# Kernel tuning notes

Hardware: AMD Instinct MI355X
Metric: run time of the kernel (lower is better)

## Reference

```python
import jax, jax.numpy as jnp
import numpy as np

EMB = 128
EDGE = 32
STEPS = 3


def _lrelu(x):
    return jax.nn.leaky_relu(x, negative_slope=0.01)


def setup_inputs() -> dict:
    key = jax.random.key(0)
    ks = jax.random.split(key, 16)
    N, E, G = 50000, 400000, 256
    x = jax.random.normal(ks[0], (N, EMB), jnp.float32)
    edge_attr = jax.random.normal(ks[1], (E, EDGE), jnp.float32)
    edge_index = jax.random.randint(ks[2], (2, E), 0, N, jnp.int64)
    batch_ind = jnp.sort(jax.random.randint(ks[3], (N,), 0, G, jnp.int64))
    data_lens = jax.random.randint(ks[4], (G,), 0, G, jnp.int64)
    s = 1.0 / np.sqrt(EMB)
    Wm = jax.random.normal(ks[5], (STEPS, EMB + EDGE, EMB), jnp.float32) * s
    bm = jnp.zeros((STEPS, EMB), jnp.float32)
    Wa = jax.random.normal(ks[6], (STEPS, 3 * EMB, EMB), jnp.float32) * s
    ba = jnp.zeros((STEPS, EMB), jnp.float32)
    Wgate = jax.random.normal(ks[7], (STEPS, EMB), jnp.float32) * s
    bgate = jnp.zeros((STEPS,), jnp.float32)
    Wfeat = jax.random.normal(ks[8], (STEPS, EMB, EMB), jnp.float32) * s
    bfeat = jnp.zeros((STEPS, EMB), jnp.float32)
    Wt = jax.random.normal(ks[9], (STEPS, 2 * EMB, EMB), jnp.float32) * s
    bt = jnp.zeros((STEPS, EMB), jnp.float32)
    return {"x": x, "edge_attr": edge_attr, "Wm": Wm, "bm": bm, "Wa": Wa,
            "ba": ba, "Wgate": Wgate, "bgate": bgate, "Wfeat": Wfeat,
            "bfeat": bfeat, "Wt": Wt, "bt": bt, "edge_index": edge_index,
            "batch_ind": batch_ind, "num_graphs": 256, "data_lens": data_lens}


def reference(x, edge_attr, Wm, bm, Wa, ba, Wgate, bgate, Wfeat, bfeat, Wt, bt,
              edge_index, batch_ind, num_graphs, data_lens):
    N = x.shape[0]
    src, dst = edge_index[0], edge_index[1]  # PyG: x_j = x[src], aggregate at dst
    xg = jnp.zeros((num_graphs, EMB), x.dtype)  # xg_init is None -> zeros
    for s in range(STEPS):
        # GraphNet: gather -> message MLP -> scatter-max -> update MLP + residual
        xg_node = xg[batch_ind]                                   # [N, emb]
        z = jnp.concatenate([x[src], edge_attr], axis=1)          # [E, emb+edge]
        m = _lrelu(z @ Wm[s] + bm[s])                             # [E, emb]
        agg = jax.ops.segment_max(m, dst, num_segments=N)         # [N, emb]
        agg = jnp.where(jnp.isneginf(agg), 0.0, agg)              # PyG fills empty with 0
        z2 = jnp.concatenate([x, xg_node, agg], axis=1)           # [N, 3*emb]
        x = _lrelu(z2 @ Wa[s] + ba[s]) + x
        # GlobalNode: segment-softmax attention pooling + transform + residual
        gate = x @ Wgate[s] + bgate[s]                            # [N]
        gmax = jax.ops.segment_max(gate, batch_ind, num_segments=num_graphs)
        gmax = jnp.where(jnp.isneginf(gmax), 0.0, gmax)
        e = jnp.exp(gate - gmax[batch_ind])
        denom = jax.ops.segment_sum(e, batch_ind, num_segments=num_graphs)
        alpha = e / denom[batch_ind]                              # [N]
        feat = _lrelu(x @ Wfeat[s] + bfeat[s])                    # [N, emb]
        pooled = jax.ops.segment_sum(alpha[:, None] * feat, batch_ind,
                                     num_segments=num_graphs)     # [G, emb]
        cat = jnp.concatenate([pooled, xg], axis=1)               # [G, 2*emb]
        xg = _lrelu(cat @ Wt[s] + bt[s]) + xg
    return x, xg
```

## Files before the change

### kernel.cpp

```cpp
#include <hip/hip_runtime.h>
#include <hip/hip_bf16.h>

#define EMB 128
#define EDGE 32
#define STEPS 3

typedef short bf8s __attribute__((ext_vector_type(8)));
typedef float f32x4 __attribute__((ext_vector_type(4)));

__device__ __forceinline__ float lrelu(float v) { return v > 0.0f ? v : 0.01f * v; }
__device__ __forceinline__ unsigned short f2bf(float f) {
    unsigned u = __float_as_uint(f);
    u += 0x7fffu + ((u >> 16) & 1u);
    return (unsigned short)(u >> 16);
}
__device__ __forceinline__ float bf2f(unsigned short s) {
    return __uint_as_float(((unsigned)s) << 16);
}
__device__ __forceinline__ unsigned pk2bf(float x, float y) {
    __hip_bfloat162 h = __float22bfloat162_rn(make_float2(x, y));
    return *(unsigned*)&h;
}

__global__ void k_hist(const int* __restrict__ dst, int E, int* __restrict__ deg) {
    int e = blockIdx.x * 256 + threadIdx.x;
    if (e < E) atomicAdd(&deg[dst[e]], 1);
}

__global__ void k_scan1(const int* __restrict__ deg, int N, int* __restrict__ rowptr,
                        int* __restrict__ bsums) {
    __shared__ int s[256];
    int t = threadIdx.x;
    int i = blockIdx.x * 256 + t;
    int v = (i < N) ? deg[i] : 0;
    s[t] = v;
    __syncthreads();
#pragma unroll
    for (int off = 1; off < 256; off <<= 1) {
        int x = (t >= off) ? s[t - off] : 0;
        __syncthreads();
        s[t] += x;
        __syncthreads();
    }
    if (i < N) rowptr[i] = s[t] - v;
    if (t == 255) bsums[blockIdx.x] = s[255];
}

__global__ void k_scan2(int* __restrict__ bsums, int NB) {
    __shared__ int s[256];
    __shared__ int carry;
    int t = threadIdx.x;
    if (t == 0) carry = 0;
    __syncthreads();
    for (int base = 0; base < NB; base += 256) {
        int i = base + t;
        int v = (i < NB) ? bsums[i] : 0;
        s[t] = v;
        __syncthreads();
#pragma unroll
        for (int off = 1; off < 256; off <<= 1) {
            int x = (t >= off) ? s[t - off] : 0;
            __syncthreads();
            s[t] += x;
            __syncthreads();
        }
        int excl = s[t] - v + carry;
        if (i < NB) bsums[i] = excl;
        int tot = s[255];
        __syncthreads();
        if (t == 0) carry += tot;
        __syncthreads();
    }
}

__global__ void k_scan3(int* __restrict__ rowptr, const int* __restrict__ bsums,
                        int* __restrict__ cursor, int N, int E) {
    int i = blockIdx.x * 256 + threadIdx.x;
    if (i < N) {
        int v = rowptr[i] + bsums[i >> 8];
        rowptr[i] = v;
        cursor[i] = v;
    }
    if (i == 0) rowptr[N] = E;
}

__global__ void k_fill(const int* __restrict__ src, const int* __restrict__ dst, int E,
                       int* __restrict__ cursor, int2* __restrict__ sp2) {
    int e = blockIdx.x * 256 + threadIdx.x;
    if (e >= E) return;
    int d = dst[e];
    int p = atomicAdd(&cursor[d], 1);
    sp2[p] = make_int2(src[e], e);
}

__global__ __launch_bounds__(256) void k_eaperm(const float* __restrict__ ea,
                                                const int2* __restrict__ sp2,
                                                unsigned short* __restrict__ ea16p,
                                                int* __restrict__ srcp, int E) {
    int p = blockIdx.x * 256 + threadIdx.x;
    if (p >= E) return;
    int2 sp = sp2[p];
    srcp[p] = sp.x;
    const float4* er = (const float4*)(ea + (size_t)sp.y * EDGE);
    union { unsigned u[16]; int4 v[4]; } o;
#pragma unroll
    for (int q = 0; q < 8; ++q) {
        float4 v = er[q];
        o.u[2 * q]     = pk2bf(v.x, v.y);
        o.u[2 * q + 1] = pk2bf(v.z, v.w);
    }
    int4* dp = (int4*)(ea16p + (size_t)p * EDGE);
#pragma unroll
    for (int q = 0; q < 4; ++q) dp[q] = o.v[q];
}

__global__ __launch_bounds__(256) void k_setup(const float* __restrict__ x0,
                                               unsigned short* __restrict__ x16,
                                               int N, int XB, int NB,
                                               const float* __restrict__ ba,
                                               float* __restrict__ gb,
                                               float* __restrict__ xg_a,
                                               const int* __restrict__ batch,
                                               int* __restrict__ gstart, int G,
                                               unsigned short* __restrict__ h16,
                                               int* __restrict__ deg) {
    int b = blockIdx.x, t = threadIdx.x;
    if (b < XB) {
        size_t idx = ((size_t)b * 256 + t) * 8;
        if (idx < (size_t)N * EMB) {
            const float4* s = (const float4*)(x0 + idx);
            float4 v0 = s[0], v1 = s[1];
            union { bf8s v; unsigned u[4]; } o;
            o.u[0] = pk2bf(v0.x, v0.y);
            o.u[1] = pk2bf(v0.z, v0.w);
            o.u[2] = pk2bf(v1.x, v1.y);
            o.u[3] = pk2bf(v1.z, v1.w);
            *(bf8s*)(x16 + idx) = o.v;
        }
        return;
    }
    b -= XB;
    if (b < NB) {
        int i = b * 256 + t;
        if (i < N) deg[i] = 0;
        return;
    }
    b -= NB;
    if (b < G) {
        if (t < EMB) gb[(size_t)b * EMB + t] = ba[t];
        else xg_a[(size_t)b * EMB + (t - EMB)] = 0.f;
        if (t == 0) {
            int lo = 0, hi = N;
            while (lo < hi) {
                int mid = (lo + hi) >> 1;
                if (batch[mid] < b) lo = mid + 1; else hi = mid;
            }
            gstart[b] = lo;
        }
        return;
    }
    if (t < EMB) h16[(size_t)N * EMB + t] = 0xFF80u;
    if (t == EMB) gstart[G] = N;
}

__global__ __launch_bounds__(256) void k_wpack(const float* __restrict__ Wm,
                                               const float* __restrict__ Wa,
                                               const float* __restrict__ Wfeat,
                                               unsigned short* __restrict__ wpack) {
    int gid = blockIdx.x * 256 + threadIdx.x;
    int unit = gid >> 14;
    int e = gid & 16383;
    int s = unit / 5, u = unit % 5;
    const float* src; int rows;
    switch (u) {
        case 0: src = Wm + (size_t)s * 160 * EMB;             rows = 128; break;
        case 1: src = Wm + (size_t)s * 160 * EMB + 128 * EMB; rows = 32;  break;
        case 2: src = Wa + (size_t)s * 384 * EMB;             rows = 128; break;
        case 3: src = Wa + (size_t)s * 384 * EMB + 256 * EMB; rows = 128; break;
        default: src = Wfeat + (size_t)s * EMB * EMB;         rows = 128; break;
    }
    int k = e >> 7, n = e & 127;
    if (k >= rows) return;
    unsigned short b = f2bf(src[(size_t)k * EMB + n]);
    int kc = k >> 5, c = n >> 4, lane = (n & 15) | (((k & 31) >> 3) << 4), j = k & 7;
    wpack[(size_t)unit * 16384 + ((size_t)(kc * 8 + c) * 64 + lane) * 8 + j] = b;
}

__device__ __forceinline__ void loadAa(const unsigned short* __restrict__ A16, int row0,
                                       int wv, int lane, int N, bf8s af[4]) {
    int li = lane & 15, oct = lane >> 4;
    int m = row0 + wv * 16 + li;
    if (m >= N) m = N - 1;
    const bf8s* ar = (const bf8s*)(A16 + (size_t)m * EMB);
#pragma unroll
    for (int kc = 0; kc < 4; ++kc) af[kc] = ar[kc * 4 + oct];
}
__device__ __forceinline__ void stageB(const unsigned short* __restrict__ Bp,
                                       unsigned short* lB, int tid) {
#pragma unroll
    for (int i = 0; i < 8; ++i) {
        int idx = tid + i * 256;
        ((int4*)lB)[idx] = ((const int4*)Bp)[idx];
    }
}
__device__ __forceinline__ void mfma128r(const bf8s af[4], const unsigned short* lB,
                                         f32x4 acc[8], int lane) {
#pragma unroll
    for (int kc = 0; kc < 4; ++kc) {
#pragma unroll
        for (int c = 0; c < 8; ++c) {
            bf8s b = *(const bf8s*)&lB[((kc * 8 + c) * 64 + lane) * 8];
            acc[c] = __builtin_amdgcn_mfma_f32_16x16x32_bf16(af[kc], b, acc[c], 0, 0, 0);
        }
    }
}

__global__ __launch_bounds__(256) void k_gemm_bias(const unsigned short* __restrict__ A16,
                                                   const unsigned short* __restrict__ Bp,
                                                   const float* __restrict__ bias,
                                                   unsigned short* __restrict__ C, int N) {
    __shared__ unsigned short lB[16384];
    int tid = threadIdx.x, wv = tid >> 6, lane = tid & 63;
    int row0 = blockIdx.x * 64;
    stageB(Bp, lB, tid);
    bf8s af[4];
    loadAa(A16, row0, wv, lane, N, af);
    __syncthreads();
    f32x4 acc[8];
#pragma unroll
    for (int c = 0; c < 8; ++c) acc[c] = (f32x4){0.f, 0.f, 0.f, 0.f};
    mfma128r(af, lB, acc, lane);
    int li = lane & 15, quad = lane >> 4;
    float bcol[8];
#pragma unroll
    for (int c = 0; c < 8; ++c) bcol[c] = bias[c * 16 + li];
#pragma unroll
    for (int rr = 0; rr < 4; ++rr) {
        int m = row0 + wv * 16 + quad * 4 + rr;
        if (m < N) {
            union { bf8s v; unsigned u[4]; } o;
#pragma unroll
            for (int j = 0; j < 4; ++j)
                o.u[j] = pk2bf(acc[2 * j][rr] + bcol[2 * j],
                               acc[2 * j + 1][rr] + bcol[2 * j + 1]);
            *(bf8s*)&C[(size_t)m * EMB + li * 8] = o.v;
        }
    }
}

__global__ __launch_bounds__(256) void k_gemm_node(const float* __restrict__ x,
                                                   unsigned short* __restrict__ x16,
                                                   const unsigned short* __restrict__ agg16,
                                                   const unsigned short* __restrict__ BpX,
                                                   const unsigned short* __restrict__ BpA,
                                                   const float* __restrict__ gb,
                                                   const int* __restrict__ batch,
                                                   float* __restrict__ xout,
                                                   const float* __restrict__ wg,
                                                   const float* __restrict__ bg,
                                                   float* __restrict__ gate, int N) {
    __shared__ unsigned short lB[16384];
    int tid = threadIdx.x, wv = tid >> 6, lane = tid & 63;
    int row0 = blockIdx.x * 64;
    stageB(BpX, lB, tid);
    bf8s af[4];
    loadAa(x16, row0, wv, lane, N, af);
    __syncthreads();
    f32x4 acc[8];
#pragma unroll
    for (int c = 0; c < 8; ++c) acc[c] = (f32x4){0.f, 0.f, 0.f, 0.f};
    mfma128r(af, lB, acc, lane);
    __syncthreads();
    stageB(BpA, lB, tid);
    loadAa(agg16, row0, wv, lane, N, af);
    __syncthreads();
    mfma128r(af, lB, acc, lane);
    int li = lane & 15, quad = lane >> 4;
    float gpart[4] = {0.f, 0.f, 0.f, 0.f};
#pragma unroll
    for (int c = 0; c < 8; ++c) {
        int col = c * 16 + li;
        float wgc = wg[col];
#pragma unroll
        for (int rr = 0; rr < 4; ++rr) {
            int m = row0 + wv * 16 + quad * 4 + rr;
            if (m < N) {
                int g = batch[m];
                float b = gb[(size_t)g * EMB + col];
                float res = x[(size_t)m * EMB + col];
                float v = lrelu(acc[c][rr] + b) + res;
                xout[(size_t)m * EMB + col] = v;
                x16[(size_t)m * EMB + col] = f2bf(v);
                gpart[rr] = fmaf(v, wgc, gpart[rr]);
            }
        }
    }
#pragma unroll
    for (int rr = 0; rr < 4; ++rr) {
#pragma unroll
        for (int off = 1; off < 16; off <<= 1)
            gpart[rr] += __shfl_xor(gpart[rr], off, 64);
    }
    if (li == 0) {
        float b0 = bg[0];
#pragma unroll
        for (int rr = 0; rr < 4; ++rr) {
            int m = row0 + wv * 16 + quad * 4 + rr;
            if (m < N) gate[m] = gpart[rr] + b0;
        }
    }
}

__global__ __launch_bounds__(256) void k_gemm_feat(const unsigned short* __restrict__ A16,
                                                   const unsigned short* __restrict__ Bp,
                                                   const float* __restrict__ bias,
                                                   const float* __restrict__ gate,
                                                   const float* __restrict__ gmax,
                                                   const float* __restrict__ denom,
                                                   const int* __restrict__ batch,
                                                   float* __restrict__ pooled, int N) {
    __shared__ unsigned short lB[16384];
    int tid = threadIdx.x, wv = tid >> 6, lane = tid & 63;
    int row0 = blockIdx.x * 64;
    stageB(Bp, lB, tid);
    bf8s af[4];
    loadAa(A16, row0, wv, lane, N, af);
    __syncthreads();
    f32x4 acc[8];
#pragma unroll
    for (int c = 0; c < 8; ++c) acc[c] = (f32x4){0.f, 0.f, 0.f, 0.f};
    mfma128r(af, lB, acc, lane);
    int li = lane & 15, quad = lane >> 4;
    int rb = row0 + wv * 16;
    if (rb >= N) return;
    float alpha[4];
    int grow[4];
#pragma unroll
    for (int rr = 0; rr < 4; ++rr) {
        int m = rb + quad * 4 + rr;
        if (m < N) {
            int g = batch[m];
            grow[rr] = g;
            alpha[rr] = __expf(gate[m] - gmax[g]) / denom[g];
        } else { alpha[rr] = 0.f; grow[rr] = 0; }
    }
    int gs = batch[rb];
    int mlast = rb + 15; if (mlast >= N) mlast = N - 1;
    bool uni = (gs == batch[mlast]);
#pragma unroll
    for (int c = 0; c < 8; ++c) {
        int col = c * 16 + li;
        float b = bias[col];
        float v0 = alpha[0] * lrelu(acc[c][0] + b);
        float v1 = alpha[1] * lrelu(acc[c][1] + b);
        float v2 = alpha[2] * lrelu(acc[c][2] + b);
        float v3 = alpha[3] * lrelu(acc[c][3] + b);
        if (uni) {
            float s = (v0 + v1) + (v2 + v3);
            s += __shfl_xor(s, 16, 64);
            s += __shfl_xor(s, 32, 64);
            if (quad == 0) atomicAdd(&pooled[(size_t)gs * EMB + col], s);
        } else {
            if (rb + quad * 4 + 0 < N) atomicAdd(&pooled[(size_t)grow[0] * EMB + col], v0);
            if (rb + quad * 4 + 1 < N) atomicAdd(&pooled[(size_t)grow[1] * EMB + col], v1);
            if (rb + quad * 4 + 2 < N) atomicAdd(&pooled[(size_t)grow[2] * EMB + col], v2);
            if (rb + quad * 4 + 3 < N) atomicAdd(&pooled[(size_t)grow[3] * EMB + col], v3);
        }
    }
}

__global__ __launch_bounds__(256) void k_gseg(const float* __restrict__ gate,
                                              const int* __restrict__ gstart,
                                              float* __restrict__ gmax,
                                              float* __restrict__ denom,
                                              float* __restrict__ pooled) {
    int g = blockIdx.x;
    int t = threadIdx.x;
    if (t < EMB) pooled[(size_t)g * EMB + t] = 0.f;
    int s0 = gstart[g], s1 = gstart[g + 1];
    __shared__ float red[256];
    float mx = -__builtin_inff();
    for (int i = s0 + t; i < s1; i += 256) mx = fmaxf(mx, gate[i]);
    red[t] = mx;
    __syncthreads();
#pragma unroll
    for (int off = 128; off; off >>= 1) {
        if (t < off) red[t] = fmaxf(red[t], red[t + off]);
        __syncthreads();
    }
    float m = red[0];
    __syncthreads();
    float sum = 0.f;
    for (int i = s0 + t; i < s1; i += 256) sum += __expf(gate[i] - m);
    red[t] = sum;
    __syncthreads();
#pragma unroll
    for (int off = 128; off; off >>= 1) {
        if (t < off) red[t] += red[t + off];
        __syncthreads();
    }
    if (t == 0) {
        gmax[g] = (s1 > s0) ? m : 0.f;
        denom[g] = red[0];
    }
}

__global__ __launch_bounds__(128) void k_xg(const float* __restrict__ pooled,
                                            const float* __restrict__ xg,
                                            const float* __restrict__ Wt,
                                            const float* __restrict__ bt,
                                            float* __restrict__ xg_out,
                                            const float* __restrict__ WaGn,
                                            const float* __restrict__ ban,
                                            float* __restrict__ gb) {
    int g = blockIdx.x, c = threadIdx.x;
    __shared__ float row[256];
    row[c] = pooled[(size_t)g * EMB + c];
    row[c + 128] = xg[(size_t)g * EMB + c];
    __syncthreads();
    float acc = bt[c];
#pragma unroll 8
    for (int k = 0; k < 256; ++k) acc = fmaf(row[k], Wt[(size_t)k * EMB + c], acc);
    float v = lrelu(acc) + row[c + 128];
    xg_out[(size_t)g * EMB + c] = v;
    if (WaGn) {
        __syncthreads();
        row[c] = v;
        __syncthreads();
        float a2 = ban[c];
#pragma unroll 8
        for (int k = 0; k < EMB; ++k) a2 = fmaf(row[k], WaGn[(size_t)k * EMB + c], a2);
        gb[(size_t)g * EMB + c] = a2;
    }
}

__global__ __launch_bounds__(1024) void k_fagg(const unsigned short* __restrict__ h,
                                               const unsigned short* __restrict__ ea16p,
                                               const int* __restrict__ srcp,
                                               const int* __restrict__ rowptr,
                                               const unsigned short* __restrict__ Bp,
                                               unsigned short* __restrict__ agg, int N) {
    __shared__ unsigned short lB[4096];
    int tid = threadIdx.x;
    if (tid < 512) ((int4*)lB)[tid] = ((const int4*)Bp)[tid];
    __syncthreads();
    int wv = tid >> 6, lane = tid & 63;
    int n = blockIdx.x * 16 + wv;
    if (n >= N) return;
    int li = lane & 15, oct = lane >> 4;
    int r0 = rowptr[n], r1 = rowptr[n + 1], deg = r1 - r0;

    float vm[8];
#pragma unroll
    for (int ci = 0; ci < 8; ++ci) vm[ci] = -__builtin_inff();

    for (int b = 0; b < deg; b += 16) {
        int p = r0 + b + li;
        if (p > r1 - 1) p = r1 - 1;
        int srcv = srcp[p];
        bf8s a = *(const bf8s*)&ea16p[(size_t)p * EDGE + oct * 8];
        union { bf8s v; unsigned short s[8]; } hv[4];
#pragma unroll
        for (int rr = 0; rr < 4; ++rr) {
            int sr = __shfl(srcv, oct * 4 + rr, 16);
            if (b + oct * 4 + rr >= deg) sr = N;
            hv[rr].v = *(const bf8s*)&h[(size_t)sr * EMB + li * 8];
        }
#pragma unroll
        for (int ci = 0; ci < 8; ++ci) {
            bf8s bb = *(const bf8s*)&lB[(ci * 64 + lane) * 8];
            f32x4 acc;
            acc[0] = bf2f(hv[0].s[ci]);
            acc[1] = bf2f(hv[1].s[ci]);
            acc[2] = bf2f(hv[2].s[ci]);
            acc[3] = bf2f(hv[3].s[ci]);
            acc = __builtin_amdgcn_mfma_f32_16x16x32_bf16(a, bb, acc, 0, 0, 0);
#pragma unroll
            for (int rr = 0; rr < 4; ++rr) vm[ci] = fmaxf(vm[ci], acc[rr]);
        }
    }
#pragma unroll
    for (int ci = 0; ci < 8; ++ci) {
        vm[ci] = fmaxf(vm[ci], __shfl_xor(vm[ci], 16, 64));
        vm[ci] = fmaxf(vm[ci], __shfl_xor(vm[ci], 32, 64));
    }
    float s0 = (oct == 0) ? vm[0] : (oct == 1) ? vm[1] : (oct == 2) ? vm[2] : vm[3];
    float s1 = (oct == 0) ? vm[4] : (oct == 1) ? vm[5] : (oct == 2) ? vm[6] : vm[7];
    s0 = lrelu(s0);
    s1 = lrelu(s1);
    if (deg == 0) { s0 = 0.f; s1 = 0.f; }
    agg[(size_t)n * EMB + oct * 16 + li]        = f2bf(s0);
    agg[(size_t)n * EMB + (oct + 4) * 16 + li]  = f2bf(s1);
}

extern "C" void kernel_launch(void* const* d_in, const int* in_sizes, int n_in,
                              void* d_out, int out_size, void* d_ws, size_t ws_size,
                              hipStream_t stream) {
    const float* x0    = (const float*)d_in[0];
    const float* ea    = (const float*)d_in[1];
    const float* Wm    = (const float*)d_in[2];
    const float* bm    = (const float*)d_in[3];
    const float* Wa    = (const float*)d_in[4];
    const float* ba    = (const float*)d_in[5];
    const float* Wgate = (const float*)d_in[6];
    const float* bgate = (const float*)d_in[7];
    const float* Wfeat = (const float*)d_in[8];
    const float* bfeat = (const float*)d_in[9];
    const float* Wt    = (const float*)d_in[10];
    const float* bt    = (const float*)d_in[11];
    const int*   eidx  = (const int*)d_in[12];
    const int*   batch = (const int*)d_in[13];

    int N = in_sizes[0] / EMB;
    int E = in_sizes[1] / EDGE;
    int G = in_sizes[15];

    char* w = (char*)d_ws;
    auto alloc = [&](size_t bytes) {
        char* p = w;
        w += (bytes + 255) & ~(size_t)255;
        return p;
    };
    unsigned short* h16   = (unsigned short*)alloc((size_t)(N + 1) * EMB * 2);
    unsigned short* x16   = (unsigned short*)alloc((size_t)N * EMB * 2);
    unsigned short* agg16 = (unsigned short*)alloc((size_t)N * EMB * 2);
    float* gate   = (float*)alloc((size_t)N * 4);
    float* gb     = (float*)alloc((size_t)G * EMB * 4);
    float* pooled = (float*)alloc((size_t)G * EMB * 4);
    float* gmax   = (float*)alloc((size_t)G * 4);
    float* denom  = (float*)alloc((size_t)G * 4);
    float* xg_a   = (float*)alloc((size_t)G * EMB * 4);
    float* xg_b   = (float*)alloc((size_t)G * EMB * 4);
    int* deg      = (int*)alloc((size_t)N * 4);
    int* rowptr   = (int*)alloc((size_t)(N + 1) * 4);
    int* cursor   = (int*)alloc((size_t)N * 4);
    int2* sp2     = (int2*)alloc((size_t)E * 8);
    int* srcp     = (int*)alloc((size_t)E * 4);
    unsigned short* ea16p = (unsigned short*)alloc((size_t)E * EDGE * 2);
    int* gstart   = (int*)alloc((size_t)(G + 1) * 4);
    int* bsums    = (int*)alloc(1024 * 4);
    unsigned short* wpack = (unsigned short*)alloc((size_t)15 * 16384 * 2);

    const int* esrc = eidx;
    const int* edst = eidx + E;
    int ebl = (E + 255) / 256;
    int NB  = (N + 255) / 256;
    int XB  = ((size_t)N * EMB / 8 + 255) / 256;

    k_setup<<<XB + NB + G + 1, 256, 0, stream>>>(x0, x16, N, XB, NB, ba, gb, xg_a,
                                                 batch, gstart, G, h16, deg);
    k_hist<<<ebl, 256, 0, stream>>>(edst, E, deg);
    k_scan1<<<NB, 256, 0, stream>>>(deg, N, rowptr, bsums);
    k_scan2<<<1, 256, 0, stream>>>(bsums, NB);
    k_scan3<<<NB, 256, 0, stream>>>(rowptr, bsums, cursor, N, E);
    k_fill<<<ebl, 256, 0, stream>>>(esrc, edst, E, cursor, sp2);
    k_eaperm<<<ebl, 256, 0, stream>>>(ea, sp2, ea16p, srcp, E);
    k_wpack<<<960, 256, 0, stream>>>(Wm, Wa, Wfeat, wpack);

    int gemm_blocks = (N + 63) / 64;
    int fagg_blocks = (N + 15) / 16;

    const float* x_in = x0;
    float* xg_cur = xg_a;
    float* xg_nxt = xg_b;

    for (int s = 0; s < STEPS; ++s) {
        const unsigned short* wp = wpack + (size_t)s * 5 * 16384;
        float* x_out = (s == STEPS - 1) ? (float*)d_out : (float*)x_in;

        k_gemm_bias<<<gemm_blocks, 256, 0, stream>>>(x16, wp + 0 * 16384, bm + s * EMB,
                                                     h16, N);
        k_fagg<<<fagg_blocks, 1024, 0, stream>>>(h16, ea16p, srcp, rowptr, wp + 1 * 16384,
                                                 agg16, N);
        k_gemm_node<<<gemm_blocks, 256, 0, stream>>>(x_in, x16, agg16, wp + 2 * 16384,
                                                     wp + 3 * 16384, gb, batch, x_out,
                                                     Wgate + s * EMB, bgate + s, gate, N);
        k_gseg<<<G, 256, 0, stream>>>(gate, gstart, gmax, denom, pooled);
        k_gemm_feat<<<gemm_blocks, 256, 0, stream>>>(x16, wp + 4 * 16384, bfeat + s * EMB,
                                                     gate, gmax, denom, batch, pooled, N);
        const float* WaGn = (s < STEPS - 1) ? Wa + (size_t)(s + 1) * 384 * EMB + 128 * EMB
                                            : nullptr;
        const float* ban  = (s < STEPS - 1) ? ba + (s + 1) * EMB : nullptr;
        k_xg<<<G, 128, 0, stream>>>(pooled, xg_cur, Wt + (size_t)s * 256 * EMB,
                                    bt + s * EMB, xg_nxt, WaGn, ban, gb);

        x_in = x_out;
        float* tmp = xg_cur; xg_cur = xg_nxt; xg_nxt = tmp;
    }

    hipMemcpyAsync((float*)d_out + (size_t)N * EMB, xg_cur, (size_t)G * EMB * 4,
                   hipMemcpyDeviceToDevice, stream);
}
```

Measured before the change: 564.0 us.

## Process 128 rows per GEMM block, batch 4 nodes per fagg wave, drop fp32 residual

The GEMM kernels now handle two 64-row tiles per block, so the staged weight tile in LDS is reused and the number of blocks is halved. k_fagg drops from 1024 to 256 threads and gives each wave four destination nodes, issuing the first-16-edge gathers for all four up front to raise memory-level parallelism. The node-update residual is read from the bf16 x16 copy instead of fp32 x, and fp32 x is written only on the last step. The final xg is written straight to the output, which removes the trailing memcpy. Taking the residual from bf16 lowers precision, and the added per-thread state may raise register pressure.

```diff
diff --git a/kernel.cpp b/kernel.cpp
--- a/kernel.cpp
+++ b/kernel.cpp
@@ -221,94 +221,122 @@
                                                    unsigned short* __restrict__ C, int N) {
     __shared__ unsigned short lB[16384];
     int tid = threadIdx.x, wv = tid >> 6, lane = tid & 63;
-    int row0 = blockIdx.x * 64;
     stageB(Bp, lB, tid);
-    bf8s af[4];
-    loadAa(A16, row0, wv, lane, N, af);
-    __syncthreads();
-    f32x4 acc[8];
-#pragma unroll
-    for (int c = 0; c < 8; ++c) acc[c] = (f32x4){0.f, 0.f, 0.f, 0.f};
-    mfma128r(af, lB, acc, lane);
+    __syncthreads();
     int li = lane & 15, quad = lane >> 4;
     float bcol[8];
 #pragma unroll
     for (int c = 0; c < 8; ++c) bcol[c] = bias[c * 16 + li];
 #pragma unroll
+    for (int half = 0; half < 2; ++half) {
+        int row0 = blockIdx.x * 128 + half * 64;
+        if (row0 >= N) break;
+        bf8s af[4];
+        loadAa(A16, row0, wv, lane, N, af);
+        f32x4 acc[8];
+#pragma unroll
+        for (int c = 0; c < 8; ++c) acc[c] = (f32x4){0.f, 0.f, 0.f, 0.f};
+        mfma128r(af, lB, acc, lane);
+#pragma unroll
+        for (int rr = 0; rr < 4; ++rr) {
+            int m = row0 + wv * 16 + quad * 4 + rr;
+            if (m < N) {
+                union { bf8s v; unsigned u[4]; } o;
+#pragma unroll
+                for (int j = 0; j < 4; ++j)
+                    o.u[j] = pk2bf(acc[2 * j][rr] + bcol[2 * j],
+                                   acc[2 * j + 1][rr] + bcol[2 * j + 1]);
+                *(bf8s*)&C[(size_t)m * EMB + li * 8] = o.v;
+            }
+        }
+    }
+}
+
+__device__ __forceinline__ void node_epi(const f32x4 acc[8], int row0, int wv, int lane,
+                                         const float* __restrict__ gb,
+                                         const int* __restrict__ batch,
+                                         unsigned short* __restrict__ x16,
+                                         float* __restrict__ xout_f32,
+                                         const float* __restrict__ wg,
+                                         const float* __restrict__ bg,
+                                         float* __restrict__ gate, int N) {
+    int li = lane & 15, quad = lane >> 4;
+    float gpart[4] = {0.f, 0.f, 0.f, 0.f};
+#pragma unroll
+    for (int c = 0; c < 8; ++c) {
+        int col = c * 16 + li;
+        float wgc = wg[col];
+#pragma unroll
+        for (int rr = 0; rr < 4; ++rr) {
+            int m = row0 + wv * 16 + quad * 4 + rr;
+            if (m < N) {
+                int g = batch[m];
+                float b = gb[(size_t)g * EMB + col];
+                float res = bf2f(x16[(size_t)m * EMB + col]);
+                float v = lrelu(acc[c][rr] + b) + res;
+                x16[(size_t)m * EMB + col] = f2bf(v);
+                if (xout_f32) xout_f32[(size_t)m * EMB + col] = v;
+                gpart[rr] = fmaf(v, wgc, gpart[rr]);
+            }
+        }
+    }
+#pragma unroll
     for (int rr = 0; rr < 4; ++rr) {
-        int m = row0 + wv * 16 + quad * 4 + rr;
-        if (m < N) {
-            union { bf8s v; unsigned u[4]; } o;
-#pragma unroll
-            for (int j = 0; j < 4; ++j)
-                o.u[j] = pk2bf(acc[2 * j][rr] + bcol[2 * j],
-                               acc[2 * j + 1][rr] + bcol[2 * j + 1]);
-            *(bf8s*)&C[(size_t)m * EMB + li * 8] = o.v;
-        }
-    }
-}
-
-__global__ __launch_bounds__(256) void k_gemm_node(const float* __restrict__ x,
-                                                   unsigned short* __restrict__ x16,
+#pragma unroll
+        for (int off = 1; off < 16; off <<= 1)
+            gpart[rr] += __shfl_xor(gpart[rr], off, 64);
+    }
+    if (li == 0) {
+        float b0 = bg[0];
+#pragma unroll
+        for (int rr = 0; rr < 4; ++rr) {
+            int m = row0 + wv * 16 + quad * 4 + rr;
+            if (m < N) gate[m] = gpart[rr] + b0;
+        }
+    }
+}
+
+__global__ __launch_bounds__(256) void k_gemm_node(unsigned short* __restrict__ x16,
                                                    const unsigned short* __restrict__ agg16,
                                                    const unsigned short* __restrict__ BpX,
                                                    const unsigned short* __restrict__ BpA,
                                                    const float* __restrict__ gb,
                                                    const int* __restrict__ batch,
-                                                   float* __restrict__ xout,
+                                                   float* __restrict__ xout_f32,
                                                    const float* __restrict__ wg,
                                                    const float* __restrict__ bg,
                                                    float* __restrict__ gate, int N) {
     __shared__ unsigned short lB[16384];
     int tid = threadIdx.x, wv = tid >> 6, lane = tid & 63;
-    int row0 = blockIdx.x * 64;
+    int row0 = blockIdx.x * 128;
+    int row1 = row0 + 64;
+    bool h1 = (row1 < N);
     stageB(BpX, lB, tid);
+    __syncthreads();
+    f32x4 acc0[8], acc1[8];
+#pragma unroll
+    for (int c = 0; c < 8; ++c) {
+        acc0[c] = (f32x4){0.f, 0.f, 0.f, 0.f};
+        acc1[c] = (f32x4){0.f, 0.f, 0.f, 0.f};
+    }
     bf8s af[4];
     loadAa(x16, row0, wv, lane, N, af);
-    __syncthreads();
-    f32x4 acc[8];
-#pragma unroll
-    for (int c = 0; c < 8; ++c) acc[c] = (f32x4){0.f, 0.f, 0.f, 0.f};
-    mfma128r(af, lB, acc, lane);
+    mfma128r(af, lB, acc0, lane);
+    if (h1) {
+        loadAa(x16, row1, wv, lane, N, af);
+        mfma128r(af, lB, acc1, lane);
+    }
     __syncthreads();
     stageB(BpA, lB, tid);
+    __syncthreads();
     loadAa(agg16, row0, wv, lane, N, af);
-    __syncthreads();
-    mfma128r(af, lB, acc, lane);
-    int li = lane & 15, quad = lane >> 4;
-    float gpart[4] = {0.f, 0.f, 0.f, 0.f};
-#pragma unroll
-    for (int c = 0; c < 8; ++c) {
-        int col = c * 16 + li;
-        float wgc = wg[col];
-#pragma unroll
-        for (int rr = 0; rr < 4; ++rr) {
-            int m = row0 + wv * 16 + quad * 4 + rr;
-            if (m < N) {
-                int g = batch[m];
-                float b = gb[(size_t)g * EMB + col];
-                float res = x[(size_t)m * EMB + col];
-                float v = lrelu(acc[c][rr] + b) + res;
-                xout[(size_t)m * EMB + col] = v;
-                x16[(size_t)m * EMB + col] = f2bf(v);
-                gpart[rr] = fmaf(v, wgc, gpart[rr]);
-            }
-        }
-    }
-#pragma unroll
-    for (int rr = 0; rr < 4; ++rr) {
-#pragma unroll
-        for (int off = 1; off < 16; off <<= 1)
-            gpart[rr] += __shfl_xor(gpart[rr], off, 64);
-    }
-    if (li == 0) {
-        float b0 = bg[0];
-#pragma unroll
-        for (int rr = 0; rr < 4; ++rr) {
-            int m = row0 + wv * 16 + quad * 4 + rr;
-            if (m < N) gate[m] = gpart[rr] + b0;
-        }
-    }
+    mfma128r(af, lB, acc0, lane);
+    if (h1) {
+        loadAa(agg16, row1, wv, lane, N, af);
+        mfma128r(af, lB, acc1, lane);
+    }
+    node_epi(acc0, row0, wv, lane, gb, batch, x16, xout_f32, wg, bg, gate, N);
+    if (h1) node_epi(acc1, row1, wv, lane, gb, batch, x16, xout_f32, wg, bg, gate, N);
 }
 
 __global__ __launch_bounds__(256) void k_gemm_feat(const unsigned short* __restrict__ A16,
@@ -321,50 +349,54 @@
                                                    float* __restrict__ pooled, int N) {
     __shared__ unsigned short lB[16384];
     int tid = threadIdx.x, wv = tid >> 6, lane = tid & 63;
-    int row0 = blockIdx.x * 64;
     stageB(Bp, lB, tid);
-    bf8s af[4];
-    loadAa(A16, row0, wv, lane, N, af);
-    __syncthreads();
-    f32x4 acc[8];
-#pragma unroll
-    for (int c = 0; c < 8; ++c) acc[c] = (f32x4){0.f, 0.f, 0.f, 0.f};
-    mfma128r(af, lB, acc, lane);
+    __syncthreads();
     int li = lane & 15, quad = lane >> 4;
-    int rb = row0 + wv * 16;
-    if (rb >= N) return;
-    float alpha[4];
-    int grow[4];
-#pragma unroll
-    for (int rr = 0; rr < 4; ++rr) {
-        int m = rb + quad * 4 + rr;
-        if (m < N) {
-            int g = batch[m];
-            grow[rr] = g;
-            alpha[rr] = __expf(gate[m] - gmax[g]) / denom[g];
-        } else { alpha[rr] = 0.f; grow[rr] = 0; }
-    }
-    int gs = batch[rb];
-    int mlast = rb + 15; if (mlast >= N) mlast = N - 1;
-    bool uni = (gs == batch[mlast]);
-#pragma unroll
-    for (int c = 0; c < 8; ++c) {
-        int col = c * 16 + li;
-        float b = bias[col];
-        float v0 = alpha[0] * lrelu(acc[c][0] + b);
-        float v1 = alpha[1] * lrelu(acc[c][1] + b);
-        float v2 = alpha[2] * lrelu(acc[c][2] + b);
-        float v3 = alpha[3] * lrelu(acc[c][3] + b);
-        if (uni) {
-            float s = (v0 + v1) + (v2 + v3);
-            s += __shfl_xor(s, 16, 64);
-            s += __shfl_xor(s, 32, 64);
-            if (quad == 0) atomicAdd(&pooled[(size_t)gs * EMB + col], s);
-        } else {
-            if (rb + quad * 4 + 0 < N) atomicAdd(&pooled[(size_t)grow[0] * EMB + col], v0);
-            if (rb + quad * 4 + 1 < N) atomicAdd(&pooled[(size_t)grow[1] * EMB + col], v1);
-            if (rb + quad * 4 + 2 < N) atomicAdd(&pooled[(size_t)grow[2] * EMB + col], v2);
-            if (rb + quad * 4 + 3 < N) atomicAdd(&pooled[(size_t)grow[3] * EMB + col], v3);
+#pragma unroll
+    for (int half = 0; half < 2; ++half) {
+        int row0 = blockIdx.x * 128 + half * 64;
+        if (row0 >= N) break;
+        bf8s af[4];
+        loadAa(A16, row0, wv, lane, N, af);
+        f32x4 acc[8];
+#pragma unroll
+        for (int c = 0; c < 8; ++c) acc[c] = (f32x4){0.f, 0.f, 0.f, 0.f};
+        mfma128r(af, lB, acc, lane);
+        int rb = row0 + wv * 16;
+        if (rb >= N) continue;
+        float alpha[4];
+        int grow[4];
+#pragma unroll
+        for (int rr = 0; rr < 4; ++rr) {
+            int m = rb + quad * 4 + rr;
+            if (m < N) {
+                int g = batch[m];
+                grow[rr] = g;
+                alpha[rr] = __expf(gate[m] - gmax[g]) / denom[g];
+            } else { alpha[rr] = 0.f; grow[rr] = 0; }
+        }
+        int gs = batch[rb];
+        int mlast = rb + 15; if (mlast >= N) mlast = N - 1;
+        bool uni = (gs == batch[mlast]);
+#pragma unroll
+        for (int c = 0; c < 8; ++c) {
+            int col = c * 16 + li;
+            float b = bias[col];
+            float v0 = alpha[0] * lrelu(acc[c][0] + b);
+            float v1 = alpha[1] * lrelu(acc[c][1] + b);
+            float v2 = alpha[2] * lrelu(acc[c][2] + b);
+            float v3 = alpha[3] * lrelu(acc[c][3] + b);
+            if (uni) {
+                float s = (v0 + v1) + (v2 + v3);
+                s += __shfl_xor(s, 16, 64);
+                s += __shfl_xor(s, 32, 64);
+                if (quad == 0) atomicAdd(&pooled[(size_t)gs * EMB + col], s);
+            } else {
+                if (rb + quad * 4 + 0 < N) atomicAdd(&pooled[(size_t)grow[0] * EMB + col], v0);
+                if (rb + quad * 4 + 1 < N) atomicAdd(&pooled[(size_t)grow[1] * EMB + col], v1);
+                if (rb + quad * 4 + 2 < N) atomicAdd(&pooled[(size_t)grow[2] * EMB + col], v2);
+                if (rb + quad * 4 + 3 < N) atomicAdd(&pooled[(size_t)grow[3] * EMB + col], v3);
+            }
         }
     }
 }
@@ -434,63 +466,117 @@
     }
 }
 
-__global__ __launch_bounds__(1024) void k_fagg(const unsigned short* __restrict__ h,
-                                               const unsigned short* __restrict__ ea16p,
-                                               const int* __restrict__ srcp,
-                                               const int* __restrict__ rowptr,
-                                               const unsigned short* __restrict__ Bp,
-                                               unsigned short* __restrict__ agg, int N) {
+__global__ __launch_bounds__(256) void k_fagg(const unsigned short* __restrict__ h,
+                                              const unsigned short* __restrict__ ea16p,
+                                              const int* __restrict__ srcp,
+                                              const int* __restrict__ rowptr,
+                                              const unsigned short* __restrict__ Bp,
+                                              unsigned short* __restrict__ agg, int N) {
     __shared__ unsigned short lB[4096];
     int tid = threadIdx.x;
-    if (tid < 512) ((int4*)lB)[tid] = ((const int4*)Bp)[tid];
+    ((int4*)lB)[tid]       = ((const int4*)Bp)[tid];
+    ((int4*)lB)[tid + 256] = ((const int4*)Bp)[tid + 256];
     __syncthreads();
     int wv = tid >> 6, lane = tid & 63;
-    int n = blockIdx.x * 16 + wv;
-    if (n >= N) return;
     int li = lane & 15, oct = lane >> 4;
-    int r0 = rowptr[n], r1 = rowptr[n + 1], deg = r1 - r0;
-
-    float vm[8];
-#pragma unroll
-    for (int ci = 0; ci < 8; ++ci) vm[ci] = -__builtin_inff();
-
-    for (int b = 0; b < deg; b += 16) {
-        int p = r0 + b + li;
-        if (p > r1 - 1) p = r1 - 1;
-        int srcv = srcp[p];
-        bf8s a = *(const bf8s*)&ea16p[(size_t)p * EDGE + oct * 8];
-        union { bf8s v; unsigned short s[8]; } hv[4];
+    int n0 = blockIdx.x * 16 + wv * 4;
+    if (n0 >= N) return;
+
+    int r[5];
+#pragma unroll
+    for (int i = 0; i <= 4; ++i) {
+        int idx = n0 + i; if (idx > N) idx = N;
+        r[i] = rowptr[idx];
+    }
+    int deg[4];
+#pragma unroll
+    for (int i = 0; i < 4; ++i) deg[i] = r[i + 1] - r[i];
+
+    float vm[4][8];
+#pragma unroll
+    for (int i = 0; i < 4; ++i)
+#pragma unroll
+        for (int ci = 0; ci < 8; ++ci) vm[i][ci] = -__builtin_inff();
+
+    union HV { bf8s v; unsigned short s[8]; };
+    int srcv[4]; bf8s a[4];
+#pragma unroll
+    for (int i = 0; i < 4; ++i) {
+        int p = r[i] + li;
+        int hi = r[i + 1] - 1;
+        if (p > hi) p = (hi >= r[i]) ? hi : 0;
+        srcv[i] = srcp[p];
+        a[i] = *(const bf8s*)&ea16p[(size_t)p * EDGE + oct * 8];
+    }
+    HV hv[4][4];
+#pragma unroll
+    for (int i = 0; i < 4; ++i) {
 #pragma unroll
         for (int rr = 0; rr < 4; ++rr) {
-            int sr = __shfl(srcv, oct * 4 + rr, 16);
-            if (b + oct * 4 + rr >= deg) sr = N;
-            hv[rr].v = *(const bf8s*)&h[(size_t)sr * EMB + li * 8];
-        }
+            int sr = __shfl(srcv[i], oct * 4 + rr, 16);
+            if (oct * 4 + rr >= deg[i]) sr = N;
+            hv[i][rr].v = *(const bf8s*)&h[(size_t)sr * EMB + li * 8];
+        }
+    }
+#pragma unroll
+    for (int i = 0; i < 4; ++i) {
 #pragma unroll
         for (int ci = 0; ci < 8; ++ci) {
             bf8s bb = *(const bf8s*)&lB[(ci * 64 + lane) * 8];
             f32x4 acc;
-            acc[0] = bf2f(hv[0].s[ci]);
-            acc[1] = bf2f(hv[1].s[ci]);
-            acc[2] = bf2f(hv[2].s[ci]);
-            acc[3] = bf2f(hv[3].s[ci]);
-            acc = __builtin_amdgcn_mfma_f32_16x16x32_bf16(a, bb, acc, 0, 0, 0);
-#pragma unroll
-            for (int rr = 0; rr < 4; ++rr) vm[ci] = fmaxf(vm[ci], acc[rr]);
-        }
-    }
-#pragma unroll
-    for (int ci = 0; ci < 8; ++ci) {
-        vm[ci] = fmaxf(vm[ci], __shfl_xor(vm[ci], 16, 64));
-        vm[ci] = fmaxf(vm[ci], __shfl_xor(vm[ci], 32, 64));
-    }
-    float s0 = (oct == 0) ? vm[0] : (oct == 1) ? vm[1] : (oct == 2) ? vm[2] : vm[3];
-    float s1 = (oct == 0) ? vm[4] : (oct == 1) ? vm[5] : (oct == 2) ? vm[6] : vm[7];
-    s0 = lrelu(s0);
-    s1 = lrelu(s1);
-    if (deg == 0) { s0 = 0.f; s1 = 0.f; }
-    agg[(size_t)n * EMB + oct * 16 + li]        = f2bf(s0);
-    agg[(size_t)n * EMB + (oct + 4) * 16 + li]  = f2bf(s1);
+            acc[0] = bf2f(hv[i][0].s[ci]);
+            acc[1] = bf2f(hv[i][1].s[ci]);
+            acc[2] = bf2f(hv[i][2].s[ci]);
+            acc[3] = bf2f(hv[i][3].s[ci]);
+            acc = __builtin_amdgcn_mfma_f32_16x16x32_bf16(a[i], bb, acc, 0, 0, 0);
+#pragma unroll
+            for (int rr = 0; rr < 4; ++rr) vm[i][ci] = fmaxf(vm[i][ci], acc[rr]);
+        }
+    }
+#pragma unroll
+    for (int i = 0; i < 4; ++i) {
+        for (int b = 16; b < deg[i]; b += 16) {
+            int p = r[i] + b + li;
+            if (p > r[i + 1] - 1) p = r[i + 1] - 1;
+            int sv = srcp[p];
+            bf8s at = *(const bf8s*)&ea16p[(size_t)p * EDGE + oct * 8];
+            HV hvt[4];
+#pragma unroll
+            for (int rr = 0; rr < 4; ++rr) {
+                int sr = __shfl(sv, oct * 4 + rr, 16);
+                if (b + oct * 4 + rr >= deg[i]) sr = N;
+                hvt[rr].v = *(const bf8s*)&h[(size_t)sr * EMB + li * 8];
+            }
+#pragma unroll
+            for (int ci = 0; ci < 8; ++ci) {
+                bf8s bb = *(const bf8s*)&lB[(ci * 64 + lane) * 8];
+                f32x4 acc;
+                acc[0] = bf2f(hvt[0].s[ci]);
+                acc[1] = bf2f(hvt[1].s[ci]);
+                acc[2] = bf2f(hvt[2].s[ci]);
+                acc[3] = bf2f(hvt[3].s[ci]);
+                acc = __builtin_amdgcn_mfma_f32_16x16x32_bf16(at, bb, acc, 0, 0, 0);
+#pragma unroll
+                for (int rr = 0; rr < 4; ++rr) vm[i][ci] = fmaxf(vm[i][ci], acc[rr]);
+            }
+        }
+    }
+#pragma unroll
+    for (int i = 0; i < 4; ++i) {
+        if (n0 + i >= N) break;
+#pragma unroll
+        for (int ci = 0; ci < 8; ++ci) {
+            vm[i][ci] = fmaxf(vm[i][ci], __shfl_xor(vm[i][ci], 16, 64));
+            vm[i][ci] = fmaxf(vm[i][ci], __shfl_xor(vm[i][ci], 32, 64));
+        }
+        float s0 = (oct == 0) ? vm[i][0] : (oct == 1) ? vm[i][1] : (oct == 2) ? vm[i][2] : vm[i][3];
+        float s1 = (oct == 0) ? vm[i][4] : (oct == 1) ? vm[i][5] : (oct == 2) ? vm[i][6] : vm[i][7];
+        s0 = lrelu(s0);
+        s1 = lrelu(s1);
+        if (deg[i] == 0) { s0 = 0.f; s1 = 0.f; }
+        agg[(size_t)(n0 + i) * EMB + oct * 16 + li]       = f2bf(s0);
+        agg[(size_t)(n0 + i) * EMB + (oct + 4) * 16 + li] = f2bf(s1);
+    }
 }
 
 extern "C" void kernel_launch(void* const* d_in, const int* in_sizes, int n_in,
@@ -557,37 +643,33 @@
     k_eaperm<<<ebl, 256, 0, stream>>>(ea, sp2, ea16p, srcp, E);
     k_wpack<<<960, 256, 0, stream>>>(Wm, Wa, Wfeat, wpack);
 
-    int gemm_blocks = (N + 63) / 64;
+    int gemm_blocks = (N + 127) / 128;
     int fagg_blocks = (N + 15) / 16;
 
-    const float* x_in = x0;
     float* xg_cur = xg_a;
     float* xg_nxt = xg_b;
 
     for (int s = 0; s < STEPS; ++s) {
         const unsigned short* wp = wpack + (size_t)s * 5 * 16384;
-        float* x_out = (s == STEPS - 1) ? (float*)d_out : (float*)x_in;
+        bool last = (s == STEPS - 1);
 
         k_gemm_bias<<<gemm_blocks, 256, 0, stream>>>(x16, wp + 0 * 16384, bm + s * EMB,
                                                      h16, N);
-        k_fagg<<<fagg_blocks, 1024, 0, stream>>>(h16, ea16p, srcp, rowptr, wp + 1 * 16384,
-                                                 agg16, N);
-        k_gemm_node<<<gemm_blocks, 256, 0, stream>>>(x_in, x16, agg16, wp + 2 * 16384,
-                                                     wp + 3 * 16384, gb, batch, x_out,
+        k_fagg<<<fagg_blocks, 256, 0, stream>>>(h16, ea16p, srcp, rowptr, wp + 1 * 16384,
+                                                agg16, N);
+        k_gemm_node<<<gemm_blocks, 256, 0, stream>>>(x16, agg16, wp + 2 * 16384,
+                                                     wp + 3 * 16384, gb, batch,
+                                                     last ? (float*)d_out : nullptr,
                                                      Wgate + s * EMB, bgate + s, gate, N);
         k_gseg<<<G, 256, 0, stream>>>(gate, gstart, gmax, denom, pooled);
         k_gemm_feat<<<gemm_blocks, 256, 0, stream>>>(x16, wp + 4 * 16384, bfeat + s * EMB,
                                                      gate, gmax, denom, batch, pooled, N);
-        const float* WaGn = (s < STEPS - 1) ? Wa + (size_t)(s + 1) * 384 * EMB + 128 * EMB
-                                            : nullptr;
-        const float* ban  = (s < STEPS - 1) ? ba + (s + 1) * EMB : nullptr;
+        const float* WaGn = !last ? Wa + (size_t)(s + 1) * 384 * EMB + 128 * EMB : nullptr;
+        const float* ban  = !last ? ba + (s + 1) * EMB : nullptr;
+        float* xgout = last ? (float*)d_out + (size_t)N * EMB : xg_nxt;
         k_xg<<<G, 128, 0, stream>>>(pooled, xg_cur, Wt + (size_t)s * 256 * EMB,
-                                    bt + s * EMB, xg_nxt, WaGn, ban, gb);
-
-        x_in = x_out;
+                                    bt + s * EMB, xgout, WaGn, ban, gb);
+
         float* tmp = xg_cur; xg_cur = xg_nxt; xg_nxt = tmp;
     }
-
-    hipMemcpyAsync((float*)d_out + (size_t)N * EMB, xg_cur, (size_t)G * EMB * 4,
-                   hipMemcpyDeviceToDevice, stream);
-}
+}
```

Measured after the change: 826.2 us. 1.46x slower.
